# Optimization experiments

Hardware: AMD Instinct MI355X
Metric: run time of the kernel (lower is better)

## Reference

```python
import jax, jax.numpy as jnp
import numpy as np

B, NO, NR = 16, 128, 16256
OD, RD = 64, 32
R_SIZES = [2 * OD + RD, 256, 256, 128]   # RelationalModel layer sizes
O_SIZES = [OD + 128, 256, 128, 3]        # ObjectModel layer sizes


def _init_mlp(key, sizes):
    params = []
    for i in range(len(sizes) - 1):
        key, k1, k2 = jax.random.split(key, 3)
        lim = 1.0 / np.sqrt(sizes[i])
        W = jax.random.uniform(k1, (sizes[i + 1], sizes[i]), minval=-lim, maxval=lim, dtype=jnp.float32)
        b = jax.random.uniform(k2, (sizes[i + 1],), minval=-lim, maxval=lim, dtype=jnp.float32)
        params += [W, b]
    return params


def setup_inputs() -> dict:
    key = jax.random.key(0)
    ks = jax.random.split(key, 6)
    objects = jax.random.normal(ks[0], (B, NO, OD), dtype=jnp.float32)
    sender_relations = jax.random.uniform(ks[1], (B, NO, NR), dtype=jnp.float32)
    receiver_relations = jax.random.uniform(ks[2], (B, NO, NR), dtype=jnp.float32)
    relation_info = jax.random.normal(ks[3], (B, NR, RD), dtype=jnp.float32)
    rW0, rb0, rW1, rb1, rW2, rb2 = _init_mlp(ks[4], R_SIZES)
    oW0, ob0, oW1, ob1, oW2, ob2 = _init_mlp(ks[5], O_SIZES)
    return dict(objects=objects, sender_relations=sender_relations,
                receiver_relations=receiver_relations, relation_info=relation_info,
                rW0=rW0, rb0=rb0, rW1=rW1, rb1=rb1, rW2=rW2, rb2=rb2,
                oW0=oW0, ob0=ob0, oW1=oW1, ob1=ob1, oW2=oW2, ob2=ob2, flag=1)


def reference(objects, sender_relations, receiver_relations, relation_info,
              rW0, rb0, rW1, rb1, rW2, rb2,
              oW0, ob0, oW1, ob1, oW2, ob2, flag):
    # flag=True path of InteractionNetwork.forward (single time-step)
    # gather: [B, NR, OD] = relations^T @ objects
    senders = jnp.einsum('bor,bod->brd', sender_relations, objects)
    receivers = jnp.einsum('bor,bod->brd', receiver_relations, objects)
    x = jnp.concatenate([senders, receivers, relation_info], axis=-1)  # [B, NR, 2*OD+RD]
    # RelationalModel: nonlinearity after EVERY layer (including last)
    h = jax.nn.relu(x @ rW0.T + rb0)
    h = jax.nn.relu(h @ rW1.T + rb1)
    effects = jax.nn.relu(h @ rW2.T + rb2)                             # [B, NR, 128]
    # scatter-sum effects back onto receiver objects
    eff_recv = jnp.einsum('bor,brd->bod', receiver_relations, effects)  # [B, NO, 128]
    y = jnp.concatenate([objects, eff_recv], axis=-1)                   # [B, NO, OD+128]
    # ObjectModel: nonlinearity on all but the last layer
    g = jax.nn.relu(y @ oW0.T + ob0)
    g = jax.nn.relu(g @ oW1.T + ob1)
    return g @ oW2.T + ob2                                              # [B, NO, 3]
```

## Files before the change

kernel.cpp:

```cpp
#include <hip/hip_runtime.h>

typedef _Float16 f16;
typedef _Float16 f16x8 __attribute__((ext_vector_type(8)));
typedef _Float16 f16x4 __attribute__((ext_vector_type(4)));
typedef float f32x4 __attribute__((ext_vector_type(4)));

#define NR_ 16256
#define NO_ 128
#define NB_ 16

__device__ __forceinline__ f32x4 MF(f16x8 a, f16x8 b, f32x4 c) {
    return __builtin_amdgcn_mfma_f32_16x16x32_f16(a, b, c, 0, 0, 0);
}

__global__ void kprep(const float* __restrict__ rW0, const float* __restrict__ rW1,
                      const float* __restrict__ rW2, const float* __restrict__ objects,
                      f16* W0b, f16* W1b, f16* W2b, f16* OT, float* er)
{
    int i = blockIdx.x * 256 + threadIdx.x, n = gridDim.x * 256;
    for (int j = i; j < 40960; j += n) W0b[j] = (f16)rW0[j];
    for (int j = i; j < 65536; j += n) W1b[j] = (f16)rW1[j];
    for (int j = i; j < 32768; j += n) W2b[j] = (f16)rW2[j];
    for (int j = i; j < 131072; j += n) {
        int b = j >> 13, rem = j & 8191, o = rem >> 6, d = rem & 63;
        OT[((size_t)b << 13) + (d << 7) + o] = (f16)objects[j];
    }
    for (int j = i; j < NB_ * 128 * 128; j += n) er[j] = 0.f;
}

template<int KSTEPS, int K>
__device__ __forceinline__ void mlp64(const f16* As, int astr, const f16* __restrict__ Wb,
                                      const float* __restrict__ bias, f16* Os, int ostr,
                                      int n0, int l15, int lq)
{
    f32x4 acc[4][2] = {};
#pragma unroll
    for (int ks = 0; ks < KSTEPS; ks++) {
        f16x8 b0 = *(const f16x8*)(Wb + (size_t)(n0 + l15) * K + ks * 32 + (lq << 3));
        f16x8 b1 = *(const f16x8*)(Wb + (size_t)(n0 + 16 + l15) * K + ks * 32 + (lq << 3));
#pragma unroll
        for (int m = 0; m < 4; m++) {
            f16x8 af = *(const f16x8*)(As + (m * 16 + l15) * astr + ks * 32 + (lq << 3));
            acc[m][0] = MF(af, b0, acc[m][0]);
            acc[m][1] = MF(af, b1, acc[m][1]);
        }
    }
    float bv0 = bias[n0 + l15], bv1 = bias[n0 + 16 + l15];
#pragma unroll
    for (int m = 0; m < 4; m++) {
        f16* d = Os + (m * 16 + (lq << 2)) * ostr;
#pragma unroll
        for (int q = 0; q < 4; q++) {
            d[q * ostr + n0 + l15]      = (f16)fmaxf(acc[m][0][q] + bv0, 0.f);
            d[q * ostr + n0 + 16 + l15] = (f16)fmaxf(acc[m][1][q] + bv1, 0.f);
        }
    }
}

__global__ __launch_bounds__(512)
void krel2(const float* __restrict__ SR, const float* __restrict__ RRg,
           const float* __restrict__ RI,
           const f16* __restrict__ W0b, const f16* __restrict__ W1b,
           const f16* __restrict__ W2b,
           const float* __restrict__ rb0, const float* __restrict__ rb1,
           const float* __restrict__ rb2,
           const f16* __restrict__ OT, float* __restrict__ er)
{
    __shared__ __align__(16) char smem[125952];
    f16* OTs = (f16*)(smem);
    f16* SRt = (f16*)(smem + 17408);
    f16* RRt = (f16*)(smem + 34816);
    f16* xs  = (f16*)(smem + 52224);
    f16* RRs = (f16*)(smem + 73728);
    f16* h2s = (f16*)(smem + 92160);
    f16* h1s = (f16*)(smem + 17408);
    f16* EtS = (f16*)(smem + 52224);

    const int b = blockIdx.y;
    const int grp = blockIdx.x;
    const int tid = threadIdx.x;
    const int lane = tid & 63;
    const int wave = tid >> 6;
    const int l15 = lane & 15;
    const int lq = lane >> 4;

    for (int c = tid; c < 1024; c += 512) {
        int d = c >> 4, ko = (c & 15) << 3;
        *(f16x8*)(OTs + d * 136 + ko) = *(const f16x8*)(OT + ((size_t)b * 64 + d) * 128 + ko);
    }

    f32x4 asc[8] = {};

    for (int t = grp; t < 254; t += 16) {
        const int r0 = t * 64;

        for (int c = tid; c < 1024; c += 512) {
            int o = c >> 3, rh = (c & 7) << 3;
            const float* ps = SR + ((size_t)b * NO_ + o) * NR_ + r0 + rh;
            const float* pr = RRg + ((size_t)b * NO_ + o) * NR_ + r0 + rh;
            float4 s0 = *(const float4*)ps, s1 = *(const float4*)(ps + 4);
            float4 q0 = *(const float4*)pr, q1 = *(const float4*)(pr + 4);
            f16* ds = SRt + rh * 136 + o;
            ds[0*136] = (f16)s0.x; ds[1*136] = (f16)s0.y; ds[2*136] = (f16)s0.z; ds[3*136] = (f16)s0.w;
            ds[4*136] = (f16)s1.x; ds[5*136] = (f16)s1.y; ds[6*136] = (f16)s1.z; ds[7*136] = (f16)s1.w;
            f16* dr = RRt + rh * 136 + o;
            dr[0*136] = (f16)q0.x; dr[1*136] = (f16)q0.y; dr[2*136] = (f16)q0.z; dr[3*136] = (f16)q0.w;
            dr[4*136] = (f16)q1.x; dr[5*136] = (f16)q1.y; dr[6*136] = (f16)q1.z; dr[7*136] = (f16)q1.w;
            f16x8 rrv;
            rrv[0] = (f16)q0.x; rrv[1] = (f16)q0.y; rrv[2] = (f16)q0.z; rrv[3] = (f16)q0.w;
            rrv[4] = (f16)q1.x; rrv[5] = (f16)q1.y; rrv[6] = (f16)q1.z; rrv[7] = (f16)q1.w;
            *(f16x8*)(RRs + o * 72 + rh) = rrv;
        }
        {
            int rr = tid >> 3, cc = (tid & 7) << 2;
            float4 v = *(const float4*)(RI + ((size_t)b * NR_ + r0 + rr) * 32 + cc);
            f16* d = xs + rr * 168 + 128 + cc;
            d[0] = (f16)v.x; d[1] = (f16)v.y; d[2] = (f16)v.z; d[3] = (f16)v.w;
        }
        __syncthreads();

        {
            const f16* At = (wave < 4) ? SRt : RRt;
            const int nf = wave & 3;
            const int xcol = (wave < 4) ? 0 : 64;
            f32x4 acc[4] = {};
#pragma unroll
            for (int ks = 0; ks < 4; ks++) {
                f16x8 bf = *(const f16x8*)(OTs + (nf * 16 + l15) * 136 + ks * 32 + (lq << 3));
#pragma unroll
                for (int m = 0; m < 4; m++) {
                    f16x8 af = *(const f16x8*)(At + (m * 16 + l15) * 136 + ks * 32 + (lq << 3));
                    acc[m] = MF(af, bf, acc[m]);
                }
            }
#pragma unroll
            for (int m = 0; m < 4; m++) {
                f16* d = xs + (m * 16 + (lq << 2)) * 168 + xcol + nf * 16 + l15;
                d[0*168] = (f16)acc[m][0]; d[1*168] = (f16)acc[m][1];
                d[2*168] = (f16)acc[m][2]; d[3*168] = (f16)acc[m][3];
            }
        }
        __syncthreads();

        mlp64<5, 160>(xs, 168, W0b, rb0, h1s, 264, wave * 32, l15, lq);
        __syncthreads();
        mlp64<8, 256>(h1s, 264, W1b, rb1, h2s, 264, wave * 32, l15, lq);
        __syncthreads();

        {
            const int n0 = wave * 16;
            const int e = n0 + l15;
            f32x4 acc[4] = {};
#pragma unroll
            for (int ks = 0; ks < 8; ks++) {
                f16x8 bf = *(const f16x8*)(W2b + (size_t)e * 256 + ks * 32 + (lq << 3));
#pragma unroll
                for (int m = 0; m < 4; m++) {
                    f16x8 af = *(const f16x8*)(h2s + (m * 16 + l15) * 264 + ks * 32 + (lq << 3));
                    acc[m] = MF(af, bf, acc[m]);
                }
            }
            float bv = rb2[e];
#pragma unroll
            for (int m = 0; m < 4; m++) {
                f16x4 pk;
#pragma unroll
                for (int q = 0; q < 4; q++) pk[q] = (f16)fmaxf(acc[m][q] + bv, 0.f);
                *(f16x4*)(EtS + e * 72 + m * 16 + (lq << 2)) = pk;
            }
        }
        __syncthreads();

        {
            const int ow = wave * 16;
#pragma unroll
            for (int ks = 0; ks < 2; ks++) {
                f16x8 af = *(const f16x8*)(RRs + (ow + l15) * 72 + ks * 32 + (lq << 3));
#pragma unroll
                for (int nf = 0; nf < 8; nf++) {
                    f16x8 bf = *(const f16x8*)(EtS + (nf * 16 + l15) * 72 + ks * 32 + (lq << 3));
                    asc[nf] = MF(af, bf, asc[nf]);
                }
            }
        }
        __syncthreads();
    }

    float* dst = er + ((size_t)b << 14);
#pragma unroll
    for (int nf = 0; nf < 8; nf++) {
        int e = nf * 16 + l15;
#pragma unroll
        for (int q = 0; q < 4; q++) {
            int o = wave * 16 + (lq << 2) + q;
            atomicAdd(dst + (size_t)o * 128 + e, asc[nf][q]);
        }
    }
}

__global__ __launch_bounds__(256)
void kobj32(const float* __restrict__ objects, const float* __restrict__ er,
            const float* __restrict__ oW0, const float* __restrict__ oW1,
            const float* __restrict__ oW2,
            const float* __restrict__ ob0, const float* __restrict__ ob1,
            const float* __restrict__ ob2, float* __restrict__ out)
{
    __shared__ float ys[8][192];
    __shared__ float h1[8][256];
    __shared__ float h2[8][128];
    const int r0 = blockIdx.x * 8;
    const int tid = threadIdx.x;

    for (int c = tid; c < 8 * 192; c += 256) {
        int rr = c / 192, k = c % 192;
        ys[rr][k] = (k < 64) ? objects[(size_t)(r0 + rr) * 64 + k]
                             : er[(size_t)(r0 + rr) * 128 + (k - 64)];
    }
    __syncthreads();
    for (int c = tid; c < 8 * 256; c += 256) {
        int rr = c >> 8, n = c & 255;
        const float* w = oW0 + (size_t)n * 192;
        float s = ob0[n];
        for (int k = 0; k < 192; k++) s += ys[rr][k] * w[k];
        h1[rr][n] = fmaxf(s, 0.f);
    }
    __syncthreads();
    for (int c = tid; c < 8 * 128; c += 256) {
        int rr = c >> 7, n = c & 127;
        const float* w = oW1 + (size_t)n * 256;
        float s = ob1[n];
        for (int k = 0; k < 256; k++) s += h1[rr][k] * w[k];
        h2[rr][n] = fmaxf(s, 0.f);
    }
    __syncthreads();
    for (int c = tid; c < 24; c += 256) {
        int rr = c / 3, j = c % 3;
        const float* w = oW2 + j * 128;
        float s = ob2[j];
        for (int k = 0; k < 128; k++) s += h2[rr][k] * w[k];
        out[(size_t)(r0 + rr) * 3 + j] = s;
    }
}

extern "C" void kernel_launch(void* const* d_in, const int* in_sizes, int n_in,
                              void* d_out, int out_size, void* d_ws, size_t ws_size,
                              hipStream_t stream)
{
    (void)in_sizes; (void)n_in; (void)out_size; (void)ws_size;
    const float* objects = (const float*)d_in[0];
    const float* SR  = (const float*)d_in[1];
    const float* RRg = (const float*)d_in[2];
    const float* RI  = (const float*)d_in[3];
    const float* rW0 = (const float*)d_in[4];
    const float* rb0 = (const float*)d_in[5];
    const float* rW1 = (const float*)d_in[6];
    const float* rb1 = (const float*)d_in[7];
    const float* rW2 = (const float*)d_in[8];
    const float* rb2 = (const float*)d_in[9];
    const float* oW0 = (const float*)d_in[10];
    const float* ob0 = (const float*)d_in[11];
    const float* oW1 = (const float*)d_in[12];
    const float* ob1 = (const float*)d_in[13];
    const float* oW2 = (const float*)d_in[14];
    const float* ob2 = (const float*)d_in[15];

    char* ws = (char*)d_ws;
    f16* W0b = (f16*)(ws + 0);
    f16* W1b = (f16*)(ws + 81920);
    f16* W2b = (f16*)(ws + 212992);
    f16* OT  = (f16*)(ws + 278528);
    float* er = (float*)(ws + 540672);

    hipLaunchKernelGGL(kprep, dim3(512), dim3(256), 0, stream,
                       rW0, rW1, rW2, objects, W0b, W1b, W2b, OT, er);
    hipLaunchKernelGGL(krel2, dim3(16, 16), dim3(512), 0, stream,
                       SR, RRg, RI, W0b, W1b, W2b, rb0, rb1, rb2, OT, er);
    hipLaunchKernelGGL(kobj32, dim3(256), dim3(256), 0, stream,
                       objects, er, oW0, oW1, oW2, ob0, ob1, ob2, (float*)d_out);
}
```

Baseline: 237.1 us.

## Prefetch next relation tile into registers and XOR-swizzle shared-memory layouts

Replaces padded shared-memory strides with XOR-swizzled layouts for every tile buffer, meant to avoid bank conflicts without padding. Changes the global load pattern so each lane reads one relation column across eight objects, which lets the transposed tile be written as vector stores. Software-prefetches the next tile's sender/receiver/relation-info values into registers before the barrier so global loads overlap the MLP compute. Costs extra registers (about 36 floats per thread) and more shared memory (139 KB), and the per-lane scalar global loads are strided by NR.

Result: slower. 787.2 us (+231.9%).

```diff
diff --git a/kernel.cpp b/kernel.cpp
--- a/kernel.cpp
+++ b/kernel.cpp
@@ -11,6 +11,14 @@
 
 __device__ __forceinline__ f32x4 MF(f16x8 a, f16x8 b, f32x4 c) {
     return __builtin_amdgcn_mfma_f32_16x16x32_f16(a, b, c, 0, 0, 0);
+}
+
+__device__ __forceinline__ int swz(int r, int o, int rs) {
+    return r * rs + ((((o >> 3) ^ r) & 7) << 3) + (o & ~7 & 63) + ((o & ~7) >> 6 << 6) + (o & 7) - (o & ~7 & 56);
+}
+__device__ __forceinline__ int swzi(int r, int o, int rs) {
+    int cb = (o >> 3) ^ (r & 7);
+    return r * rs + (cb << 3) + (o & 7);
 }
 
 __global__ void kprep(const float* __restrict__ rW0, const float* __restrict__ rW1,
@@ -28,10 +36,10 @@
     for (int j = i; j < NB_ * 128 * 128; j += n) er[j] = 0.f;
 }
 
-template<int KSTEPS, int K>
-__device__ __forceinline__ void mlp64(const f16* As, int astr, const f16* __restrict__ Wb,
-                                      const float* __restrict__ bias, f16* Os, int ostr,
-                                      int n0, int l15, int lq)
+template<int KSTEPS, int K, int AS, int OS>
+__device__ __forceinline__ void mlp64s(const f16* As, const f16* __restrict__ Wb,
+                                       const float* __restrict__ bias, f16* Os,
+                                       int n0, int l15, int lq)
 {
     f32x4 acc[4][2] = {};
 #pragma unroll
@@ -40,7 +48,7 @@
         f16x8 b1 = *(const f16x8*)(Wb + (size_t)(n0 + 16 + l15) * K + ks * 32 + (lq << 3));
 #pragma unroll
         for (int m = 0; m < 4; m++) {
-            f16x8 af = *(const f16x8*)(As + (m * 16 + l15) * astr + ks * 32 + (lq << 3));
+            f16x8 af = *(const f16x8*)(As + swzi(m * 16 + l15, ks * 32 + (lq << 3), AS));
             acc[m][0] = MF(af, b0, acc[m][0]);
             acc[m][1] = MF(af, b1, acc[m][1]);
         }
@@ -48,17 +56,17 @@
     float bv0 = bias[n0 + l15], bv1 = bias[n0 + 16 + l15];
 #pragma unroll
     for (int m = 0; m < 4; m++) {
-        f16* d = Os + (m * 16 + (lq << 2)) * ostr;
 #pragma unroll
         for (int q = 0; q < 4; q++) {
-            d[q * ostr + n0 + l15]      = (f16)fmaxf(acc[m][0][q] + bv0, 0.f);
-            d[q * ostr + n0 + 16 + l15] = (f16)fmaxf(acc[m][1][q] + bv1, 0.f);
+            int row = m * 16 + (lq << 2) + q;
+            Os[swzi(row, n0 + l15, OS)]      = (f16)fmaxf(acc[m][0][q] + bv0, 0.f);
+            Os[swzi(row, n0 + 16 + l15, OS)] = (f16)fmaxf(acc[m][1][q] + bv1, 0.f);
         }
     }
 }
 
 __global__ __launch_bounds__(512)
-void krel2(const float* __restrict__ SR, const float* __restrict__ RRg,
+void krel3(const float* __restrict__ SR, const float* __restrict__ RRg,
            const float* __restrict__ RI,
            const f16* __restrict__ W0b, const f16* __restrict__ W1b,
            const f16* __restrict__ W2b,
@@ -66,15 +74,15 @@
            const float* __restrict__ rb2,
            const f16* __restrict__ OT, float* __restrict__ er)
 {
-    __shared__ __align__(16) char smem[125952];
+    __shared__ __align__(16) char smem[139264];
     f16* OTs = (f16*)(smem);
-    f16* SRt = (f16*)(smem + 17408);
-    f16* RRt = (f16*)(smem + 34816);
-    f16* xs  = (f16*)(smem + 52224);
-    f16* RRs = (f16*)(smem + 73728);
-    f16* h2s = (f16*)(smem + 92160);
-    f16* h1s = (f16*)(smem + 17408);
-    f16* EtS = (f16*)(smem + 52224);
+    f16* SRt = (f16*)(smem + 16384);
+    f16* RRt = (f16*)(smem + 32768);
+    f16* RRs = (f16*)(smem + 49152);
+    f16* xs  = (f16*)(smem + 65536);
+    f16* h2s = (f16*)(smem + 90112);
+    f16* EtS = (f16*)(smem + 122880);
+    f16* h1s = (f16*)(smem + 16384);
 
     const int b = blockIdx.y;
     const int grp = blockIdx.x;
@@ -85,38 +93,57 @@
     const int lq = lane >> 4;
 
     for (int c = tid; c < 1024; c += 512) {
-        int d = c >> 4, ko = (c & 15) << 3;
-        *(f16x8*)(OTs + d * 136 + ko) = *(const f16x8*)(OT + ((size_t)b * 64 + d) * 128 + ko);
+        int d = c >> 4, cb8 = (c & 15) << 3;
+        f16x8 v = *(const f16x8*)(OT + ((size_t)b * 64 + d) * 128 + cb8);
+        *(f16x8*)(OTs + swzi(d, cb8, 128)) = v;
     }
 
     f32x4 asc[8] = {};
+    float psr[16], prr[16], pri4[4];
+    const size_t sbase = (size_t)b * NO_ * NR_;
+
+    auto issue = [&](int t) {
+        const float* bs = SR + sbase + t * 64 + lane;
+        const float* br = RRg + sbase + t * 64 + lane;
+#pragma unroll
+        for (int p = 0; p < 2; p++)
+#pragma unroll
+            for (int j = 0; j < 8; j++) {
+                int o = ((wave + (p << 3)) << 3) + j;
+                psr[(p << 3) + j] = bs[(size_t)o * NR_];
+                prr[(p << 3) + j] = br[(size_t)o * NR_];
+            }
+        const float* bi = RI + ((size_t)b * NR_ + t * 64 + (tid >> 3)) * 32 + ((tid & 7) << 2);
+        float4 v = *(const float4*)bi;
+        pri4[0] = v.x; pri4[1] = v.y; pri4[2] = v.z; pri4[3] = v.w;
+    };
+
+    issue(grp);
 
     for (int t = grp; t < 254; t += 16) {
-        const int r0 = t * 64;
-
-        for (int c = tid; c < 1024; c += 512) {
-            int o = c >> 3, rh = (c & 7) << 3;
-            const float* ps = SR + ((size_t)b * NO_ + o) * NR_ + r0 + rh;
-            const float* pr = RRg + ((size_t)b * NO_ + o) * NR_ + r0 + rh;
-            float4 s0 = *(const float4*)ps, s1 = *(const float4*)(ps + 4);
-            float4 q0 = *(const float4*)pr, q1 = *(const float4*)(pr + 4);
-            f16* ds = SRt + rh * 136 + o;
-            ds[0*136] = (f16)s0.x; ds[1*136] = (f16)s0.y; ds[2*136] = (f16)s0.z; ds[3*136] = (f16)s0.w;
-            ds[4*136] = (f16)s1.x; ds[5*136] = (f16)s1.y; ds[6*136] = (f16)s1.z; ds[7*136] = (f16)s1.w;
-            f16* dr = RRt + rh * 136 + o;
-            dr[0*136] = (f16)q0.x; dr[1*136] = (f16)q0.y; dr[2*136] = (f16)q0.z; dr[3*136] = (f16)q0.w;
-            dr[4*136] = (f16)q1.x; dr[5*136] = (f16)q1.y; dr[6*136] = (f16)q1.z; dr[7*136] = (f16)q1.w;
-            f16x8 rrv;
-            rrv[0] = (f16)q0.x; rrv[1] = (f16)q0.y; rrv[2] = (f16)q0.z; rrv[3] = (f16)q0.w;
-            rrv[4] = (f16)q1.x; rrv[5] = (f16)q1.y; rrv[6] = (f16)q1.z; rrv[7] = (f16)q1.w;
-            *(f16x8*)(RRs + o * 72 + rh) = rrv;
+#pragma unroll
+        for (int p = 0; p < 2; p++) {
+            int cb8 = (wave + (p << 3)) << 3;
+            f16x8 s8, r8;
+#pragma unroll
+            for (int j = 0; j < 8; j++) {
+                s8[j] = (f16)psr[(p << 3) + j];
+                r8[j] = (f16)prr[(p << 3) + j];
+            }
+            *(f16x8*)(SRt + swzi(lane, cb8, 128)) = s8;
+            *(f16x8*)(RRt + swzi(lane, cb8, 128)) = r8;
+#pragma unroll
+            for (int j = 0; j < 8; j++)
+                RRs[swzi(cb8 + j, lane, 64)] = r8[j];
         }
         {
-            int rr = tid >> 3, cc = (tid & 7) << 2;
-            float4 v = *(const float4*)(RI + ((size_t)b * NR_ + r0 + rr) * 32 + cc);
-            f16* d = xs + rr * 168 + 128 + cc;
-            d[0] = (f16)v.x; d[1] = (f16)v.y; d[2] = (f16)v.z; d[3] = (f16)v.w;
-        }
+            int rr = tid >> 3, c0 = 128 + ((tid & 7) << 2);
+            f16x4 h4;
+            h4[0] = (f16)pri4[0]; h4[1] = (f16)pri4[1];
+            h4[2] = (f16)pri4[2]; h4[3] = (f16)pri4[3];
+            *(f16x4*)(xs + swzi(rr, c0, 192)) = h4;
+        }
+        if (t + 16 < 254) issue(t + 16);
         __syncthreads();
 
         {
@@ -126,37 +153,35 @@
             f32x4 acc[4] = {};
 #pragma unroll
             for (int ks = 0; ks < 4; ks++) {
-                f16x8 bf = *(const f16x8*)(OTs + (nf * 16 + l15) * 136 + ks * 32 + (lq << 3));
+                f16x8 bf = *(const f16x8*)(OTs + swzi(nf * 16 + l15, (ks << 5) + (lq << 3), 128));
 #pragma unroll
                 for (int m = 0; m < 4; m++) {
-                    f16x8 af = *(const f16x8*)(At + (m * 16 + l15) * 136 + ks * 32 + (lq << 3));
+                    f16x8 af = *(const f16x8*)(At + swzi(m * 16 + l15, (ks << 5) + (lq << 3), 128));
                     acc[m] = MF(af, bf, acc[m]);
                 }
             }
 #pragma unroll
-            for (int m = 0; m < 4; m++) {
-                f16* d = xs + (m * 16 + (lq << 2)) * 168 + xcol + nf * 16 + l15;
-                d[0*168] = (f16)acc[m][0]; d[1*168] = (f16)acc[m][1];
-                d[2*168] = (f16)acc[m][2]; d[3*168] = (f16)acc[m][3];
-            }
-        }
-        __syncthreads();
-
-        mlp64<5, 160>(xs, 168, W0b, rb0, h1s, 264, wave * 32, l15, lq);
-        __syncthreads();
-        mlp64<8, 256>(h1s, 264, W1b, rb1, h2s, 264, wave * 32, l15, lq);
+            for (int m = 0; m < 4; m++)
+#pragma unroll
+                for (int q = 0; q < 4; q++)
+                    xs[swzi(m * 16 + (lq << 2) + q, xcol + nf * 16 + l15, 192)] = (f16)acc[m][q];
+        }
+        __syncthreads();
+
+        mlp64s<5, 160, 192, 256>(xs, W0b, rb0, h1s, wave * 32, l15, lq);
+        __syncthreads();
+        mlp64s<8, 256, 256, 256>(h1s, W1b, rb1, h2s, wave * 32, l15, lq);
         __syncthreads();
 
         {
-            const int n0 = wave * 16;
-            const int e = n0 + l15;
+            const int e = (wave << 4) + l15;
             f32x4 acc[4] = {};
 #pragma unroll
             for (int ks = 0; ks < 8; ks++) {
-                f16x8 bf = *(const f16x8*)(W2b + (size_t)e * 256 + ks * 32 + (lq << 3));
+                f16x8 bf = *(const f16x8*)(W2b + (size_t)e * 256 + (ks << 5) + (lq << 3));
 #pragma unroll
                 for (int m = 0; m < 4; m++) {
-                    f16x8 af = *(const f16x8*)(h2s + (m * 16 + l15) * 264 + ks * 32 + (lq << 3));
+                    f16x8 af = *(const f16x8*)(h2s + swzi(m * 16 + l15, (ks << 5) + (lq << 3), 256));
                     acc[m] = MF(af, bf, acc[m]);
                 }
             }
@@ -166,19 +191,19 @@
                 f16x4 pk;
 #pragma unroll
                 for (int q = 0; q < 4; q++) pk[q] = (f16)fmaxf(acc[m][q] + bv, 0.f);
-                *(f16x4*)(EtS + e * 72 + m * 16 + (lq << 2)) = pk;
+                *(f16x4*)(EtS + swzi(e, (m << 4) + (lq << 2), 64)) = pk;
             }
         }
         __syncthreads();
 
         {
-            const int ow = wave * 16;
+            const int ow = wave << 4;
 #pragma unroll
             for (int ks = 0; ks < 2; ks++) {
-                f16x8 af = *(const f16x8*)(RRs + (ow + l15) * 72 + ks * 32 + (lq << 3));
+                f16x8 af = *(const f16x8*)(RRs + swzi(ow + l15, (ks << 5) + (lq << 3), 64));
 #pragma unroll
                 for (int nf = 0; nf < 8; nf++) {
-                    f16x8 bf = *(const f16x8*)(EtS + (nf * 16 + l15) * 72 + ks * 32 + (lq << 3));
+                    f16x8 bf = *(const f16x8*)(EtS + swzi((nf << 4) + l15, (ks << 5) + (lq << 3), 64));
                     asc[nf] = MF(af, bf, asc[nf]);
                 }
             }
@@ -189,10 +214,10 @@
     float* dst = er + ((size_t)b << 14);
 #pragma unroll
     for (int nf = 0; nf < 8; nf++) {
-        int e = nf * 16 + l15;
+        int e = (nf << 4) + l15;
 #pragma unroll
         for (int q = 0; q < 4; q++) {
-            int o = wave * 16 + (lq << 2) + q;
+            int o = (wave << 4) + (lq << 2) + q;
             atomicAdd(dst + (size_t)o * 128 + e, asc[nf][q]);
         }
     }
@@ -273,7 +298,7 @@
 
     hipLaunchKernelGGL(kprep, dim3(512), dim3(256), 0, stream,
                        rW0, rW1, rW2, objects, W0b, W1b, W2b, OT, er);
-    hipLaunchKernelGGL(krel2, dim3(16, 16), dim3(512), 0, stream,
+    hipLaunchKernelGGL(krel3, dim3(16, 16), dim3(512), 0, stream,
                        SR, RRg, RI, W0b, W1b, W2b, rb0, rb1, rb2, OT, er);
     hipLaunchKernelGGL(kobj32, dim3(256), dim3(256), 0, stream,
                        objects, er, oW0, oW1, oW2, ob0, ob1, ob2, (float*)d_out);
```
